# Optimization experiments

Hardware: AMD Instinct MI355X
Metric: run time of the kernel (lower is better)

## Reference

```python
import jax, jax.numpy as jnp
import numpy as np

D_MODEL = 1024
NUM_TILES = 64
TPC = 8                      # tiles_per_cluster
NUM_CLUSTERS = NUM_TILES // TPC
GRID = 16
COMP_H = 256                 # compress hidden = d_model // 4
NUM_KNOTS = 8
EPS_LN = 1e-5


def setup_inputs() -> dict:
    key = jax.random.key(0)
    ks = jax.random.split(key, 12)
    B, T = 4, 4096
    x = jax.random.normal(ks[0], (B, T, D_MODEL), dtype=jnp.float32)
    signatures_raw = jax.random.normal(ks[1], (NUM_TILES, D_MODEL), dtype=jnp.float32) * 0.5
    knot_values = jax.nn.sigmoid(jnp.linspace(-3.0, 3.0, NUM_KNOTS).astype(jnp.float32))
    temperature = jnp.ones((1,), dtype=jnp.float32)
    # compress: Linear(d,comp_h) -> GELU -> Linear(comp_h,2) -> Tanh
    compress_w1 = jax.random.normal(ks[2], (D_MODEL, COMP_H), dtype=jnp.float32) * (1.0 / np.sqrt(D_MODEL))
    compress_b1 = jnp.zeros((COMP_H,), dtype=jnp.float32)
    compress_w2 = jax.random.normal(ks[3], (COMP_H, 2), dtype=jnp.float32) * (1.0 / np.sqrt(COMP_H))
    compress_b2 = jnp.zeros((2,), dtype=jnp.float32)
    # per-tile magnitude splines: Linear(2,grid) -> ReLU -> Linear(grid,1)
    spline_w1 = jax.random.normal(ks[4], (NUM_TILES, 2, GRID), dtype=jnp.float32) * (1.0 / np.sqrt(2.0))
    spline_b1 = jnp.zeros((NUM_TILES, GRID), dtype=jnp.float32)
    spline_w2 = jax.random.normal(ks[5], (NUM_TILES, GRID, 1), dtype=jnp.float32) * (1.0 / np.sqrt(GRID))
    spline_b2 = jnp.zeros((NUM_TILES, 1), dtype=jnp.float32)
    directions = jax.random.normal(ks[6], (NUM_TILES, D_MODEL), dtype=jnp.float32) * 0.02
    norm_gamma = jnp.ones((D_MODEL,), dtype=jnp.float32)
    norm_beta = jnp.zeros((D_MODEL,), dtype=jnp.float32)
    output_scale = jnp.ones((1,), dtype=jnp.float32) * 0.1
    return dict(x=x, signatures_raw=signatures_raw, knot_values=knot_values,
                temperature=temperature, compress_w1=compress_w1, compress_b1=compress_b1,
                compress_w2=compress_w2, compress_b2=compress_b2, spline_w1=spline_w1,
                spline_b1=spline_b1, spline_w2=spline_w2, spline_b2=spline_b2,
                directions=directions, norm_gamma=norm_gamma, norm_beta=norm_beta,
                output_scale=output_scale)


def _calibrate(scores, knots, temperature):
    # ScoreCalibrationSpline: sigmoid -> linear interpolation over knots
    K = knots.shape[0]
    normalized = jax.nn.sigmoid(scores / (temperature[0] + 1e-6))
    idx_float = normalized * (K - 1)
    idx_low = jnp.clip(idx_float.astype(jnp.int32), 0, K - 2)
    idx_high = idx_low + 1
    t = idx_float - idx_low.astype(scores.dtype)
    val_low = knots[idx_low]
    val_high = knots[idx_high]
    return val_low + t * (val_high - val_low)


def _forward(x, signatures_raw, knot_values, temperature, compress_w1, compress_b1,
             compress_w2, compress_b2, spline_w1, spline_b1, spline_w2, spline_b2,
             directions, norm_gamma, norm_beta, output_scale):
    B, T, D = x.shape
    xf = x.reshape(-1, D)  # [N, D]

    # ternary quantized signatures with straight-through estimator
    q = jnp.where(signatures_raw > 0.3, 1.0,
                  jnp.where(signatures_raw < -0.3, -1.0, 0.0)).astype(signatures_raw.dtype)
    sigs = signatures_raw + jax.lax.stop_gradient(q - signatures_raw)  # [NT, D]

    # hierarchical routing: cluster signatures = sign(mean of member sigs)
    cluster_sigs = jnp.sign(sigs.reshape(NUM_CLUSTERS, TPC, D).mean(axis=1))  # [NC, D]
    cluster_scores = xf @ cluster_sigs.T                                       # [N, NC]
    cluster_gates = _calibrate(cluster_scores, knot_values, temperature)
    cluster_idx = jnp.argmax(cluster_gates, axis=-1)                           # [N]

    # within-cluster tile selection (clusters are contiguous blocks of tiles)
    tile_scores = xf @ sigs.T                                                  # [N, NT]
    tile_gates = _calibrate(tile_scores, knot_values, temperature)
    gates_by_cluster = tile_gates.reshape(-1, NUM_CLUSTERS, TPC)
    sel_gates = jnp.take_along_axis(gates_by_cluster, cluster_idx[:, None, None],
                                    axis=1)[:, 0, :]                            # [N, TPC]
    local_idx = jnp.argmax(sel_gates, axis=-1)
    tile_idx = cluster_idx * TPC + local_idx                                    # [N]

    # compress to 2D spline coordinates
    h = jax.nn.gelu(xf @ compress_w1 + compress_b1, approximate=False)
    comp = jnp.tanh(h @ compress_w2 + compress_b2)                              # [N, 2]

    # batched per-token tiny spline MLP (gather selected tile's weights)
    w1 = spline_w1[tile_idx]                                                    # [N, 2, G]
    b1 = spline_b1[tile_idx]                                                    # [N, G]
    hh = jax.nn.relu(jnp.einsum('ni,nig->ng', comp, w1) + b1)                   # [N, G]
    w2 = spline_w2[tile_idx]                                                    # [N, G, 1]
    b2 = spline_b2[tile_idx]                                                    # [N, 1]
    mag = jnp.einsum('ng,ngo->no', hh, w2) + b2                                 # [N, 1]

    ffn_out = mag * directions[tile_idx] * output_scale[0]                      # [N, D]

    # residual + LayerNorm (dropout in eval mode = identity)
    y = xf + ffn_out
    mu = y.mean(axis=-1, keepdims=True)
    var = ((y - mu) ** 2).mean(axis=-1, keepdims=True)
    y = (y - mu) / jnp.sqrt(var + EPS_LN) * norm_gamma + norm_beta
    return y.reshape(B, T, D)


def reference(x, signatures_raw, knot_values, temperature, compress_w1, compress_b1,
              compress_w2, compress_b2, spline_w1, spline_b1, spline_w2, spline_b2,
              directions, norm_gamma, norm_beta, output_scale):
    return _forward(x, signatures_raw, knot_values, temperature, compress_w1, compress_b1,
                    compress_w2, compress_b2, spline_w1, spline_b1, spline_w2, spline_b2,
                    directions, norm_gamma, norm_beta, output_scale)
```

## Files before the change

kernel.cpp:

```cpp
#include <hip/hip_runtime.h>
#include <hip/hip_bf16.h>
#include <cmath>

#define N_TOK 16384
#define DM    1024
#define CH    256
#define SGRID 16
#define NTP   24

typedef __attribute__((ext_vector_type(8))) short short8;
typedef __attribute__((ext_vector_type(4))) float floatx4;

__device__ __forceinline__ unsigned short f2bf(float f) {
  union { float f; unsigned int u; } v; v.f = f;
  unsigned int r = v.u + 0x7FFFu + ((v.u >> 16) & 1u);
  return (unsigned short)(r >> 16);
}

__device__ __forceinline__ short8 cvt8(float4 u, float4 v) {
  union { short8 s; __hip_bfloat162 h[4]; } r;
  r.h[0] = __float22bfloat162_rn(make_float2(u.x, u.y));
  r.h[1] = __float22bfloat162_rn(make_float2(u.z, u.w));
  r.h[2] = __float22bfloat162_rn(make_float2(v.x, v.y));
  r.h[3] = __float22bfloat162_rn(make_float2(v.z, v.w));
  return r.s;
}

__device__ __forceinline__ float calibrate(float s, const float* __restrict__ kn, float temp_eff) {
  float nrm = 1.0f / (1.0f + expf(-s / temp_eff));
  float idxf = nrm * 7.0f;
  int il = (int)idxf; if (il > 6) il = 6;
  float tt = idxf - (float)il;
  float lo = kn[il], hi = kn[il + 1];
  return lo + tt * (hi - lo);
}

__global__ __launch_bounds__(256) void prep_kernel(
    const float* __restrict__ sig_raw, const float* __restrict__ w1,
    unsigned short* __restrict__ wsB) {
  __shared__ float Wt[32][260];
  __shared__ float St[64][33];
  int kk = blockIdx.x, tid = threadIdx.x;
  {
    int r = tid >> 3, c0 = (tid & 7) * 32;
    const float* src = w1 + (size_t)(kk * 32 + r) * CH + c0;
#pragma unroll
    for (int i = 0; i < 8; ++i)
      *(float4*)(&Wt[r][c0 + 4 * i]) = *(const float4*)(src + 4 * i);
  }
  {
    int t = tid >> 2, c0 = (tid & 3) * 8;
    const float* src = sig_raw + (size_t)t * DM + kk * 32 + c0;
#pragma unroll
    for (int i = 0; i < 8; ++i) {
      float rr = src[i];
      St[t][c0 + i] = (rr > 0.3f) ? 1.f : ((rr < -0.3f) ? -1.f : 0.f);
    }
  }
  __syncthreads();
#pragma unroll
  for (int i = 0; i < 4; ++i) {
    int idx = i * 256 + tid;
    int nt = idx >> 6, lane = idx & 63;
    int q = lane >> 4, l = lane & 15;
    short8 v;
#pragma unroll
    for (int j = 0; j < 8; ++j) v[j] = (short)f2bf(Wt[q * 8 + j][nt * 16 + l]);
    *(short8*)(wsB + ((size_t)(kk * NTP + nt) * 64 + lane) * 8) = v;
  }
#pragma unroll
  for (int i = 0; i < 2; ++i) {
    int idx = i * 256 + tid;
    if (idx < 320) {
      int nt = 16 + (idx >> 6), lane = idx & 63;
      int q = lane >> 4, l = lane & 15;
      int n = nt * 16 + l;
      short8 v;
#pragma unroll
      for (int j = 0; j < 8; ++j) {
        int kl = q * 8 + j;
        float val = 0.f;
        if (n < 264) {
          float s = 0.f;
#pragma unroll
          for (int m = 0; m < 8; ++m) s += St[(n - 256) * 8 + m][kl];
          val = (s > 0.f) ? 1.f : ((s < 0.f) ? -1.f : 0.f);
        } else if (n < 328) {
          val = St[n - 264][kl];
        }
        v[j] = (short)f2bf(val);
      }
      *(short8*)(wsB + ((size_t)(kk * NTP + nt) * 64 + lane) * 8) = v;
    }
  }
}

#define LOADK(kk, bv, av)                                                   \
  {                                                                         \
    const char* bp = bBase + (size_t)(kk) * (NTP * 1024);                   \
    _Pragma("unroll") for (int s = 0; s < 6; ++s)                           \
        bv[s] = *(const short8*)(bp + s * 4096);                            \
    const float* ap = aBase + (kk) * 32;                                    \
    av[0] = *(const float4*)(ap);                                           \
    av[1] = *(const float4*)(ap + 4);                                       \
  }

#define COMPUTE(bv, av)                                                     \
  {                                                                         \
    short8 aa = cvt8(av[0], av[1]);                                         \
    _Pragma("unroll") for (int s = 0; s < 6; ++s)                           \
      acc[s] = __builtin_amdgcn_mfma_f32_16x16x32_bf16(aa, bv[s], acc[s], 0, 0, 0); \
  }

__global__ __launch_bounds__(1024, 4) void fused_kernel(
    const float* __restrict__ x, const unsigned short* __restrict__ wsB,
    const float* __restrict__ b1, const float* __restrict__ w2,
    const float* __restrict__ b2, const float* __restrict__ knots,
    const float* __restrict__ temperature, const float* __restrict__ sw1,
    const float* __restrict__ sb1, const float* __restrict__ sw2,
    const float* __restrict__ sb2, const float* __restrict__ dirs,
    const float* __restrict__ gma, const float* __restrict__ bta,
    const float* __restrict__ oscale, float* __restrict__ out) {
  __shared__ float Ssc[64][81];
  __shared__ float Psh[4][4][16][2];
  __shared__ float ScaleS[64];
  __shared__ int   TidxS[64];

  int tid = threadIdx.x;
  int wave = tid >> 6, lane = tid & 63, quad = lane >> 4, l15 = lane & 15;
  int w3 = wave & 3, h = wave >> 2;
  int m0 = blockIdx.x * 64;

  floatx4 acc[6];
#pragma unroll
  for (int s = 0; s < 6; ++s) acc[s] = (floatx4){0.f, 0.f, 0.f, 0.f};

  const char* bBase = (const char*)wsB + w3 * 1024 + lane * 16;
  const float* aBase = x + (size_t)(m0 + h * 16 + l15) * DM + quad * 8;

  short8 bA[6], bB_[6];
  float4 aA[2], aB_[2];
  LOADK(0, bA, aA);
#pragma unroll 1
  for (int kk = 0; kk < 30; kk += 2) {
    LOADK(kk + 1, bB_, aB_);
    COMPUTE(bA, aA);
    LOADK(kk + 2, bA, aA);
    COMPUTE(bB_, aB_);
  }
  LOADK(31, bB_, aB_);
  COMPUTE(bA, aA);
  COMPUTE(bB_, aB_);

#pragma unroll
  for (int r = 0; r < 4; ++r) {
    int row = h * 16 + quad * 4 + r;
    Ssc[row][w3 * 16 + l15] = acc[4][r];
    if (w3 == 0) Ssc[row][64 + l15] = acc[5][r];
  }

  float p0[4] = {0.f, 0.f, 0.f, 0.f}, p1[4] = {0.f, 0.f, 0.f, 0.f};
#pragma unroll
  for (int s = 0; s < 4; ++s) {
    int col = (w3 + 4 * s) * 16 + l15;
    float b1c = b1[col], w20 = w2[2 * col], w21 = w2[2 * col + 1];
#pragma unroll
    for (int r = 0; r < 4; ++r) {
      float hh = acc[s][r] + b1c;
      hh = 0.5f * hh * (1.0f + erff(hh * 0.7071067811865475f));
      p0[r] += hh * w20;
      p1[r] += hh * w21;
    }
  }
#pragma unroll
  for (int m = 1; m < 16; m <<= 1)
#pragma unroll
    for (int r = 0; r < 4; ++r) {
      p0[r] += __shfl_xor(p0[r], m);
      p1[r] += __shfl_xor(p1[r], m);
    }
  if (l15 == 0) {
#pragma unroll
    for (int r = 0; r < 4; ++r) {
      Psh[h][w3][quad * 4 + r][0] = p0[r];
      Psh[h][w3][quad * 4 + r][1] = p1[r];
    }
  }
  __syncthreads();

  if (tid < 64) {
    int row = tid, h2 = row >> 4, r16 = row & 15;
    float s0 = b2[0], s1 = b2[1];
#pragma unroll
    for (int j = 0; j < 4; ++j) {
      s0 += Psh[h2][j][r16][0];
      s1 += Psh[h2][j][r16][1];
    }
    float c0 = tanhf(s0), c1 = tanhf(s1);

    float temp_eff = temperature[0] + 1e-6f;
    int cid = 0; float best = -1e30f;
#pragma unroll
    for (int c = 0; c < 8; ++c) {
      float g = calibrate(Ssc[row][c], knots, temp_eff);
      if (g > best) { best = g; cid = c; }
    }
    int lidx = 0; best = -1e30f;
#pragma unroll
    for (int j = 0; j < 8; ++j) {
      float g = calibrate(Ssc[row][8 + cid * 8 + j], knots, temp_eff);
      if (g > best) { best = g; lidx = j; }
    }
    int t = cid * 8 + lidx;

    float mag = sb2[t];
#pragma unroll
    for (int g2 = 0; g2 < SGRID; ++g2) {
      float hv = c0 * sw1[t * 32 + g2] + c1 * sw1[t * 32 + 16 + g2] + sb1[t * 16 + g2];
      hv = fmaxf(hv, 0.f);
      mag += hv * sw2[t * 16 + g2];
    }
    ScaleS[row] = mag * oscale[0];
    TidxS[row] = t;
  }
  __syncthreads();

  float4 g4[4], be4[4];
#pragma unroll
  for (int i = 0; i < 4; ++i) {
    g4[i] = *(const float4*)(gma + 4 * lane + 256 * i);
    be4[i] = *(const float4*)(bta + 4 * lane + 256 * i);
  }
#pragma unroll 1
  for (int rr = 0; rr < 4; ++rr) {
    int row = wave * 4 + rr;
    float scale = ScaleS[row];
    const float* xr = x + (size_t)(m0 + row) * DM;
    const float* dr = dirs + (size_t)TidxS[row] * DM;
    float4 fv[4];
    float ssum = 0.f, ssq = 0.f;
#pragma unroll
    for (int i = 0; i < 4; ++i) {
      float4 xv = *(const float4*)(xr + 4 * lane + 256 * i);
      float4 d4 = *(const float4*)(dr + 4 * lane + 256 * i);
      fv[i].x = xv.x + scale * d4.x;
      fv[i].y = xv.y + scale * d4.y;
      fv[i].z = xv.z + scale * d4.z;
      fv[i].w = xv.w + scale * d4.w;
      ssum += fv[i].x + fv[i].y + fv[i].z + fv[i].w;
      ssq += fv[i].x * fv[i].x + fv[i].y * fv[i].y + fv[i].z * fv[i].z + fv[i].w * fv[i].w;
    }
#pragma unroll
    for (int m = 1; m < 64; m <<= 1) {
      ssum += __shfl_xor(ssum, m);
      ssq += __shfl_xor(ssq, m);
    }
    float mu = ssum * (1.0f / 1024.0f);
    float var = ssq * (1.0f / 1024.0f) - mu * mu;
    float inv = rsqrtf(var + 1e-5f);
    float* orow = out + (size_t)(m0 + row) * DM;
#pragma unroll
    for (int i = 0; i < 4; ++i) {
      float4 o;
      o.x = (fv[i].x - mu) * inv * g4[i].x + be4[i].x;
      o.y = (fv[i].y - mu) * inv * g4[i].y + be4[i].y;
      o.z = (fv[i].z - mu) * inv * g4[i].z + be4[i].z;
      o.w = (fv[i].w - mu) * inv * g4[i].w + be4[i].w;
      *(float4*)(orow + 4 * lane + 256 * i) = o;
    }
  }
}

extern "C" void kernel_launch(void* const* d_in, const int* in_sizes, int n_in,
                              void* d_out, int out_size, void* d_ws, size_t ws_size,
                              hipStream_t stream) {
  const float* x      = (const float*)d_in[0];
  const float* sigraw = (const float*)d_in[1];
  const float* knots  = (const float*)d_in[2];
  const float* temp   = (const float*)d_in[3];
  const float* cw1    = (const float*)d_in[4];
  const float* cb1    = (const float*)d_in[5];
  const float* cw2    = (const float*)d_in[6];
  const float* cb2    = (const float*)d_in[7];
  const float* sw1    = (const float*)d_in[8];
  const float* sb1    = (const float*)d_in[9];
  const float* sw2    = (const float*)d_in[10];
  const float* sb2    = (const float*)d_in[11];
  const float* dirs   = (const float*)d_in[12];
  const float* gma    = (const float*)d_in[13];
  const float* bta    = (const float*)d_in[14];
  const float* oscale = (const float*)d_in[15];
  float* out = (float*)d_out;

  unsigned short* wsB = (unsigned short*)d_ws;

  hipLaunchKernelGGL(prep_kernel, dim3(32), dim3(256), 0, stream,
                     sigraw, cw1, wsB);
  hipLaunchKernelGGL(fused_kernel, dim3(N_TOK / 64), dim3(1024), 0, stream,
                     x, wsB, cb1, cw2, cb2, knots, temp,
                     sw1, sb1, sw2, sb2, dirs, gma, bta, oscale, out);
}
```

Baseline: 212.0 us.

## Stage compress weights in LDS via async global_load_lds double buffering

Each k-step's weight tile (21 chunks, dropping the 3 unused padding chunks) is now copied once per block into a double-buffered LDS area with global_load_lds, instead of every wave loading its own B fragments straight from global memory. Waves then read their B operands from LDS. To fit the LDS budget the block shrinks to 32 tokens and 512 threads, and the grid doubles. The aim is to cut redundant L2 traffic and register pressure for B. The cost is two __syncthreads per k-step, and the code relies on the async LDS writes having completed by the barrier. The rest of the epilogue, which is not fully visible, must also agree with the 32-row tile.

```diff
diff --git a/kernel.cpp b/kernel.cpp
--- a/kernel.cpp
+++ b/kernel.cpp
@@ -95,24 +95,40 @@
   }
 }
 
-#define LOADK(kk, bv, av)                                                   \
+
+#define DMAB(kk, buf)                                                       \
   {                                                                         \
-    const char* bp = bBase + (size_t)(kk) * (NTP * 1024);                   \
-    _Pragma("unroll") for (int s = 0; s < 6; ++s)                           \
-        bv[s] = *(const short8*)(bp + s * 4096);                            \
+    const char* g = gB + (size_t)(kk) * (NTP * 1024);                       \
+    _Pragma("unroll") for (int i = 0; i < 3; ++i) {                         \
+      int c = i * 8 + wave;                                                 \
+      if (c < 21)                                                           \
+        __builtin_amdgcn_global_load_lds(                                   \
+            (const __attribute__((address_space(1))) void*)(g + c * 1024 + lane * 16), \
+            (__attribute__((address_space(3))) void*)((buf) + c * 1024), 16, 0, 0); \
+    }                                                                       \
+  }
+
+#define LOADA(kk, av)                                                       \
+  {                                                                         \
     const float* ap = aBase + (kk) * 32;                                    \
     av[0] = *(const float4*)(ap);                                           \
     av[1] = *(const float4*)(ap + 4);                                       \
   }
 
-#define COMPUTE(bv, av)                                                     \
+#define COMPUTE(buf, av)                                                    \
   {                                                                         \
     short8 aa = cvt8(av[0], av[1]);                                         \
-    _Pragma("unroll") for (int s = 0; s < 6; ++s)                           \
-      acc[s] = __builtin_amdgcn_mfma_f32_16x16x32_bf16(aa, bv[s], acc[s], 0, 0, 0); \
-  }
-
-__global__ __launch_bounds__(1024, 4) void fused_kernel(
+    _Pragma("unroll") for (int s = 0; s < 5; ++s) {                         \
+      short8 b = *(const short8*)((buf) + (w3 + 4 * s) * 1024 + lane * 16); \
+      acc[s] = __builtin_amdgcn_mfma_f32_16x16x32_bf16(aa, b, acc[s], 0, 0, 0); \
+    }                                                                       \
+    if (w3 == 0) {                                                          \
+      short8 b = *(const short8*)((buf) + 20 * 1024 + lane * 16);           \
+      acc[5] = __builtin_amdgcn_mfma_f32_16x16x32_bf16(aa, b, acc[5], 0, 0, 0); \
+    }                                                                       \
+  }
+
+__global__ __launch_bounds__(512, 4) void fused_kernel(
     const float* __restrict__ x, const unsigned short* __restrict__ wsB,
     const float* __restrict__ b1, const float* __restrict__ w2,
     const float* __restrict__ b2, const float* __restrict__ knots,
@@ -121,36 +137,38 @@
     const float* __restrict__ sb2, const float* __restrict__ dirs,
     const float* __restrict__ gma, const float* __restrict__ bta,
     const float* __restrict__ oscale, float* __restrict__ out) {
-  __shared__ float Ssc[64][81];
-  __shared__ float Psh[4][4][16][2];
-  __shared__ float ScaleS[64];
-  __shared__ int   TidxS[64];
+  __shared__ char BshRaw[2 * 21504];
+  __shared__ float Ssc[32][81];
+  __shared__ float Psh[2][4][16][2];
+  __shared__ float ScaleS[32];
+  __shared__ int   TidxS[32];
 
   int tid = threadIdx.x;
   int wave = tid >> 6, lane = tid & 63, quad = lane >> 4, l15 = lane & 15;
   int w3 = wave & 3, h = wave >> 2;
-  int m0 = blockIdx.x * 64;
+  int m0 = blockIdx.x * 32;
 
   floatx4 acc[6];
 #pragma unroll
   for (int s = 0; s < 6; ++s) acc[s] = (floatx4){0.f, 0.f, 0.f, 0.f};
 
-  const char* bBase = (const char*)wsB + w3 * 1024 + lane * 16;
+  const char* gB = (const char*)wsB;
   const float* aBase = x + (size_t)(m0 + h * 16 + l15) * DM + quad * 8;
-
-  short8 bA[6], bB_[6];
+  char* buf0 = BshRaw;
+  char* buf1 = BshRaw + 21504;
+
   float4 aA[2], aB_[2];
-  LOADK(0, bA, aA);
+  DMAB(0, buf0);
+  LOADA(0, aA);
 #pragma unroll 1
-  for (int kk = 0; kk < 30; kk += 2) {
-    LOADK(kk + 1, bB_, aB_);
-    COMPUTE(bA, aA);
-    LOADK(kk + 2, bA, aA);
-    COMPUTE(bB_, aB_);
-  }
-  LOADK(31, bB_, aB_);
-  COMPUTE(bA, aA);
-  COMPUTE(bB_, aB_);
+  for (int kk = 0; kk < 32; kk += 2) {
+    __syncthreads();
+    if (kk + 1 < 32) { DMAB(kk + 1, buf1); LOADA(kk + 1, aB_); }
+    COMPUTE(buf0, aA);
+    __syncthreads();
+    if (kk + 2 < 32) { DMAB(kk + 2, buf0); LOADA(kk + 2, aA); }
+    COMPUTE(buf1, aB_);
+  }
 
 #pragma unroll
   for (int r = 0; r < 4; ++r) {
@@ -188,7 +206,7 @@
   }
   __syncthreads();
 
-  if (tid < 64) {
+  if (tid < 32) {
     int row = tid, h2 = row >> 4, r16 = row & 15;
     float s0 = b2[0], s1 = b2[1];
 #pragma unroll
@@ -296,7 +314,7 @@
 
   hipLaunchKernelGGL(prep_kernel, dim3(32), dim3(256), 0, stream,
                      sigraw, cw1, wsB);
-  hipLaunchKernelGGL(fused_kernel, dim3(N_TOK / 64), dim3(1024), 0, stream,
+  hipLaunchKernelGGL(fused_kernel, dim3(N_TOK / 32), dim3(512), 0, stream,
                      x, wsB, cb1, cw2, cb2, knots, temp,
                      sw1, sb1, sw2, sb2, dirs, gma, bta, oscale, out);
 }
```

After: 196.7 us. -7.2%, faster.

## Stage x tile as bf16 in LDS and reuse it for GEMM and LayerNorm

Applied to the files above, without the earlier changes.

Each block now cooperatively loads its 32-row x tile once, converts it to bf16 and stores it in a swizzled shared-memory buffer. Both the MFMA A-operand reads and the residual/LayerNorm pass read from that buffer, removing the second global read of x and the per-iteration fp32-to-bf16 conversion. Blocks shrink to 32 rows and 512 threads, and the sixth B-fragment load and MFMA are restricted to the one wave that needs them. The trade-offs are a 64 KB LDS footprint per block, which limits occupancy, and a bf16-rounded x in the residual, which loses accuracy in the output.

```diff
diff --git a/kernel.cpp b/kernel.cpp
--- a/kernel.cpp
+++ b/kernel.cpp
@@ -24,6 +24,10 @@
   r.h[2] = __float22bfloat162_rn(make_float2(v.x, v.y));
   r.h[3] = __float22bfloat162_rn(make_float2(v.z, v.w));
   return r.s;
+}
+
+__device__ __forceinline__ float bf2f(unsigned short b) {
+  union { unsigned int u; float f; } v; v.u = ((unsigned int)b) << 16; return v.f;
 }
 
 __device__ __forceinline__ float calibrate(float s, const float* __restrict__ kn, float temp_eff) {
@@ -95,24 +99,25 @@
   }
 }
 
-#define LOADK(kk, bv, av)                                                   \
+
+#define LOADK(kk, bv, aav)                                                  \
   {                                                                         \
     const char* bp = bBase + (size_t)(kk) * (NTP * 1024);                   \
-    _Pragma("unroll") for (int s = 0; s < 6; ++s)                           \
+    _Pragma("unroll") for (int s = 0; s < 5; ++s)                           \
         bv[s] = *(const short8*)(bp + s * 4096);                            \
-    const float* ap = aBase + (kk) * 32;                                    \
-    av[0] = *(const float4*)(ap);                                           \
-    av[1] = *(const float4*)(ap + 4);                                       \
-  }
-
-#define COMPUTE(bv, av)                                                     \
+    if (w3 == 0) bv[5] = *(const short8*)(bp + 20 * 1024);                  \
+    aav = *(const short8*)(Xsh + arow + (((unsigned)((kk) * 4 + quad) ^ sw) << 3)); \
+  }
+
+#define COMPUTE(bv, aav)                                                    \
   {                                                                         \
-    short8 aa = cvt8(av[0], av[1]);                                         \
-    _Pragma("unroll") for (int s = 0; s < 6; ++s)                           \
-      acc[s] = __builtin_amdgcn_mfma_f32_16x16x32_bf16(aa, bv[s], acc[s], 0, 0, 0); \
-  }
-
-__global__ __launch_bounds__(1024, 4) void fused_kernel(
+    _Pragma("unroll") for (int s = 0; s < 5; ++s)                           \
+      acc[s] = __builtin_amdgcn_mfma_f32_16x16x32_bf16(aav, bv[s], acc[s], 0, 0, 0); \
+    if (w3 == 0)                                                            \
+      acc[5] = __builtin_amdgcn_mfma_f32_16x16x32_bf16(aav, bv[5], acc[5], 0, 0, 0); \
+  }
+
+__global__ __launch_bounds__(512, 4) void fused_kernel(
     const float* __restrict__ x, const unsigned short* __restrict__ wsB,
     const float* __restrict__ b1, const float* __restrict__ w2,
     const float* __restrict__ b2, const float* __restrict__ knots,
@@ -121,25 +126,40 @@
     const float* __restrict__ sb2, const float* __restrict__ dirs,
     const float* __restrict__ gma, const float* __restrict__ bta,
     const float* __restrict__ oscale, float* __restrict__ out) {
-  __shared__ float Ssc[64][81];
-  __shared__ float Psh[4][4][16][2];
-  __shared__ float ScaleS[64];
-  __shared__ int   TidxS[64];
+  __shared__ unsigned short Xsh[32 * 1024];
+  __shared__ float Ssc[32][73];
+  __shared__ float Psh[2][4][16][2];
+  __shared__ float ScaleS[32];
+  __shared__ int   TidxS[32];
 
   int tid = threadIdx.x;
   int wave = tid >> 6, lane = tid & 63, quad = lane >> 4, l15 = lane & 15;
   int w3 = wave & 3, h = wave >> 2;
-  int m0 = blockIdx.x * 64;
+  int m0 = blockIdx.x * 32;
+
+  {
+    const float* base = x + (size_t)m0 * DM;
+#pragma unroll
+    for (int i2 = 0; i2 < 8; ++i2) {
+      int cg = tid + 512 * i2;
+      float4 p = *(const float4*)(base + cg * 8);
+      float4 q = *(const float4*)(base + cg * 8 + 4);
+      int row = cg >> 7, cir = cg & 127;
+      int pos = cir ^ (row & 7);
+      *(short8*)(Xsh + row * 1024 + pos * 8) = cvt8(p, q);
+    }
+  }
+  __syncthreads();
 
   floatx4 acc[6];
 #pragma unroll
   for (int s = 0; s < 6; ++s) acc[s] = (floatx4){0.f, 0.f, 0.f, 0.f};
 
   const char* bBase = (const char*)wsB + w3 * 1024 + lane * 16;
-  const float* aBase = x + (size_t)(m0 + h * 16 + l15) * DM + quad * 8;
-
-  short8 bA[6], bB_[6];
-  float4 aA[2], aB_[2];
+  int arow = (h * 16 + l15) * 1024;
+  unsigned sw = (unsigned)(l15 & 7);
+
+  short8 bA[6], bB_[6], aA, aB_;
   LOADK(0, bA, aA);
 #pragma unroll 1
   for (int kk = 0; kk < 30; kk += 2) {
@@ -156,7 +176,7 @@
   for (int r = 0; r < 4; ++r) {
     int row = h * 16 + quad * 4 + r;
     Ssc[row][w3 * 16 + l15] = acc[4][r];
-    if (w3 == 0) Ssc[row][64 + l15] = acc[5][r];
+    if (w3 == 0 && l15 < 8) Ssc[row][64 + l15] = acc[5][r];
   }
 
   float p0[4] = {0.f, 0.f, 0.f, 0.f}, p1[4] = {0.f, 0.f, 0.f, 0.f};
@@ -188,7 +208,7 @@
   }
   __syncthreads();
 
-  if (tid < 64) {
+  if (tid < 32) {
     int row = tid, h2 = row >> 4, r16 = row & 15;
     float s0 = b2[0], s1 = b2[1];
 #pragma unroll
@@ -225,30 +245,31 @@
   }
   __syncthreads();
 
-  float4 g4[4], be4[4];
-#pragma unroll
-  for (int i = 0; i < 4; ++i) {
-    g4[i] = *(const float4*)(gma + 4 * lane + 256 * i);
-    be4[i] = *(const float4*)(bta + 4 * lane + 256 * i);
-  }
 #pragma unroll 1
   for (int rr = 0; rr < 4; ++rr) {
     int row = wave * 4 + rr;
+    int r7 = row & 7;
     float scale = ScaleS[row];
-    const float* xr = x + (size_t)(m0 + row) * DM;
-    const float* dr = dirs + (size_t)TidxS[row] * DM;
-    float4 fv[4];
+    const float* dr = dirs + (size_t)TidxS[row] * DM + lane * 16;
+    const unsigned short* xrow = Xsh + row * 1024;
+    short8 h0 = *(const short8*)(xrow + (unsigned)((2 * lane) ^ r7) * 8);
+    short8 h1 = *(const short8*)(xrow + (unsigned)((2 * lane + 1) ^ r7) * 8);
+    float fv[16];
     float ssum = 0.f, ssq = 0.f;
 #pragma unroll
     for (int i = 0; i < 4; ++i) {
-      float4 xv = *(const float4*)(xr + 4 * lane + 256 * i);
-      float4 d4 = *(const float4*)(dr + 4 * lane + 256 * i);
-      fv[i].x = xv.x + scale * d4.x;
-      fv[i].y = xv.y + scale * d4.y;
-      fv[i].z = xv.z + scale * d4.z;
-      fv[i].w = xv.w + scale * d4.w;
-      ssum += fv[i].x + fv[i].y + fv[i].z + fv[i].w;
-      ssq += fv[i].x * fv[i].x + fv[i].y * fv[i].y + fv[i].z * fv[i].z + fv[i].w * fv[i].w;
+      float4 d4 = *(const float4*)(dr + 4 * i);
+      float xa = bf2f((unsigned short)((i < 2 ? h0[i * 4 + 0] : h1[(i - 2) * 4 + 0])));
+      float xb = bf2f((unsigned short)((i < 2 ? h0[i * 4 + 1] : h1[(i - 2) * 4 + 1])));
+      float xc = bf2f((unsigned short)((i < 2 ? h0[i * 4 + 2] : h1[(i - 2) * 4 + 2])));
+      float xd = bf2f((unsigned short)((i < 2 ? h0[i * 4 + 3] : h1[(i - 2) * 4 + 3])));
+      fv[4 * i + 0] = xa + scale * d4.x;
+      fv[4 * i + 1] = xb + scale * d4.y;
+      fv[4 * i + 2] = xc + scale * d4.z;
+      fv[4 * i + 3] = xd + scale * d4.w;
+      ssum += fv[4 * i + 0] + fv[4 * i + 1] + fv[4 * i + 2] + fv[4 * i + 3];
+      ssq += fv[4 * i + 0] * fv[4 * i + 0] + fv[4 * i + 1] * fv[4 * i + 1]
+           + fv[4 * i + 2] * fv[4 * i + 2] + fv[4 * i + 3] * fv[4 * i + 3];
     }
 #pragma unroll
     for (int m = 1; m < 64; m <<= 1) {
@@ -258,15 +279,19 @@
     float mu = ssum * (1.0f / 1024.0f);
     float var = ssq * (1.0f / 1024.0f) - mu * mu;
     float inv = rsqrtf(var + 1e-5f);
-    float* orow = out + (size_t)(m0 + row) * DM;
+    float* orow = out + (size_t)(m0 + row) * DM + lane * 16;
+    const float* gp = gma + lane * 16;
+    const float* bp2 = bta + lane * 16;
 #pragma unroll
     for (int i = 0; i < 4; ++i) {
+      float4 g4 = *(const float4*)(gp + 4 * i);
+      float4 b4 = *(const float4*)(bp2 + 4 * i);
       float4 o;
-      o.x = (fv[i].x - mu) * inv * g4[i].x + be4[i].x;
-      o.y = (fv[i].y - mu) * inv * g4[i].y + be4[i].y;
-      o.z = (fv[i].z - mu) * inv * g4[i].z + be4[i].z;
-      o.w = (fv[i].w - mu) * inv * g4[i].w + be4[i].w;
-      *(float4*)(orow + 4 * lane + 256 * i) = o;
+      o.x = (fv[4 * i + 0] - mu) * inv * g4.x + b4.x;
+      o.y = (fv[4 * i + 1] - mu) * inv * g4.y + b4.y;
+      o.z = (fv[4 * i + 2] - mu) * inv * g4.z + b4.z;
+      o.w = (fv[4 * i + 3] - mu) * inv * g4.w + b4.w;
+      *(float4*)(orow + 4 * i) = o;
     }
   }
 }
@@ -296,7 +321,7 @@
 
   hipLaunchKernelGGL(prep_kernel, dim3(32), dim3(256), 0, stream,
                      sigraw, cw1, wsB);
-  hipLaunchKernelGGL(fused_kernel, dim3(N_TOK / 64), dim3(1024), 0, stream,
+  hipLaunchKernelGGL(fused_kernel, dim3(N_TOK / 32), dim3(512), 0, stream,
                      x, wsB, cb1, cw2, cb2, knots, temp,
                      sw1, sb1, sw2, sb2, dirs, gma, bta, oscale, out);
 }
```

After: 184.2 us. 1.15x faster.
